# Kernel tuning notes

Measured on AMD Instinct MI355X. Metric: run time of the kernel, lower is better.

## Reference

```python
import jax, jax.numpy as jnp
import numpy as np

DIM, DEPTH, HEADS, DIM_HEAD, MLP = 256, 4, 8, 32, 1024
INNER = HEADS * DIM_HEAD  # 256
B, N = 16, 4096
EPS = 1e-5


def _ln(x, g, b):
    m = jnp.mean(x, axis=-1, keepdims=True)
    v = jnp.mean(jnp.square(x - m), axis=-1, keepdims=True)
    return (x - m) * jax.lax.rsqrt(v + EPS) * g + b


def setup_inputs() -> dict:
    key = jax.random.key(0)
    ks = jax.random.split(key, 16)
    s_in = 1.0 / np.sqrt(DIM)
    s_inner = 1.0 / np.sqrt(INNER)
    s_mlp = 1.0 / np.sqrt(MLP)
    return {
        "x": jax.random.normal(ks[0], (B, N, DIM), jnp.float32),
        "patch_indices": jax.random.randint(ks[1], (B, 2), 0, 64, jnp.int32),
        "data": jnp.zeros((1,), jnp.float32),
        "scale": jnp.array([64, 64], jnp.int32),
        "Wq": jax.random.normal(ks[2], (DEPTH, DIM, INNER), jnp.float32) * s_in,
        "Wk": jax.random.normal(ks[3], (DEPTH, DIM, INNER), jnp.float32) * s_in,
        "Wv": jax.random.normal(ks[4], (DEPTH, DIM, INNER), jnp.float32) * s_in,
        "Wo": jax.random.normal(ks[5], (DEPTH, INNER, DIM), jnp.float32) * s_inner,
        "bo": jnp.zeros((DEPTH, DIM), jnp.float32),
        "ln_g": jnp.ones((DEPTH, DIM), jnp.float32),
        "ln_b": jnp.zeros((DEPTH, DIM), jnp.float32),
        "W1": jax.random.normal(ks[6], (DEPTH, DIM, MLP), jnp.float32) * s_in,
        "b1": jnp.zeros((DEPTH, MLP), jnp.float32),
        "W2": jax.random.normal(ks[7], (DEPTH, MLP, DIM), jnp.float32) * s_mlp,
        "b2": jnp.zeros((DEPTH, DIM), jnp.float32),
        "lnf_g": jnp.ones((DIM,), jnp.float32),
        "lnf_b": jnp.zeros((DIM,), jnp.float32),
    }


def reference(x, patch_indices, data, scale, Wq, Wk, Wv, Wo, bo, ln_g, ln_b,
              W1, b1, W2, b2, lnf_g, lnf_b):
    b, n, dim = x.shape
    attn_scale = DIM_HEAD ** (-0.5)
    # flat index of the center pixel per batch element: row * h_patch + col
    idx = (patch_indices[:, 0] * scale[1] + patch_indices[:, 1]).astype(jnp.int32)  # [b]
    bidx = jnp.arange(b)
    for l in range(DEPTH):
        sel = x[bidx, idx]                                  # [b, dim] gathered center token
        q = (sel @ Wq[l]).reshape(b, HEADS, DIM_HEAD)       # [b, h, d]
        k = (x @ Wk[l]).reshape(b, n, HEADS, DIM_HEAD)      # [b, n, h, d]
        v = (x @ Wv[l]).reshape(b, n, HEADS, DIM_HEAD)
        dots = jnp.einsum('bhd,bnhd->bhn', q, k) * attn_scale
        attn = jax.nn.softmax(dots, axis=-1)                # [b, h, n]
        out = jnp.einsum('bhn,bnhd->bhd', attn, v).reshape(b, INNER)
        out = out @ Wo[l] + bo[l]                           # [b, dim]
        # vectorized scatter of the single attended token back into a zero tensor
        x = jnp.zeros_like(x).at[bidx, idx].set(out) + x
        # FeedForward: LN -> Linear -> GELU (exact) -> Linear, plus residual
        h = jax.nn.gelu(_ln(x, ln_g[l], ln_b[l]) @ W1[l] + b1[l], approximate=False)
        x = h @ W2[l] + b2[l] + x
    return _ln(x, lnf_g, lnf_b)
```

## Files before the change

### kernel.cpp

```cpp
#include <hip/hip_runtime.h>
#include <hip/hip_bf16.h>
#include <math.h>

#define B 16
#define NTOK 4096
#define DIM 256
#define DEPTH 4
#define HEADS 8
#define DH 32
#define INNER 256
#define MLPD 1024
#define EPS 1e-5f

typedef _Float16 half8 __attribute__((ext_vector_type(8)));
typedef _Float16 half4v __attribute__((ext_vector_type(4)));
typedef float f32x4 __attribute__((ext_vector_type(4)));

__device__ __forceinline__ float gelu_fast(float v) {
    const float z = fabsf(v) * 0.70710678118654752440f;
    const float t = __builtin_amdgcn_rcpf(1.f + 0.3275911f * z);
    const float poly = t*(0.254829592f + t*(-0.284496736f +
                      t*(1.421413741f + t*(-1.453152027f + t*1.061405429f))));
    const float e = __expf(-z*z);
    const float erfv = copysignf(1.f - poly * e, v);
    return 0.5f * v * (1.f + erfv);
}

__global__ __launch_bounds__(256) void pack_w(
        const float* __restrict__ in, _Float16* __restrict__ out, int K, int C)
{
    in  += (size_t)blockIdx.z * K * C;
    out += (size_t)blockIdx.z * K * C;
    __shared__ float t[32][65];
    const int tid = threadIdx.x;
    const int c0 = blockIdx.x * 64, k0 = blockIdx.y * 32;
    #pragma unroll
    for (int i = 0; i < 8; ++i) {
        int flat = tid + 256*i;
        int kk = flat >> 6, ccl = flat & 63;
        t[kk][ccl] = in[(size_t)(k0 + kk)*C + c0 + ccl];
    }
    __syncthreads();
    const int lane = tid & 63, ctl = tid >> 6;
    const int ccl = ctl*16 + (lane & 15);
    const int kb = (lane >> 4) * 8;
    half8 v;
    #pragma unroll
    for (int i = 0; i < 8; ++i) v[i] = (_Float16)t[kb + i][ccl];
    size_t off = ((size_t)((c0 >> 4) + ctl) * (K/32) + (k0 >> 5)) * 64 + lane;
    *((half8*)out + off) = v;
}

__global__ __launch_bounds__(256) void attn_prep(
        const float* __restrict__ x, const int* __restrict__ pidx,
        const int* __restrict__ scale,
        const float* __restrict__ Wq, float* __restrict__ qbuf)
{
    const int b = blockIdx.x;
    const int tid = threadIdx.x;
    __shared__ float sel[DIM];
    const int idx = pidx[b*2 + 0] * scale[1] + pidx[b*2 + 1];
    sel[tid] = x[(size_t)b*NTOK*DIM + (size_t)idx*DIM + tid];
    __syncthreads();
    float acc = 0.f;
    #pragma unroll 4
    for (int c = 0; c < DIM; ++c) acc += sel[c] * Wq[c*INNER + tid];
    qbuf[b*DIM + tid] = acc;
}

__global__ __launch_bounds__(256) void qk_kernel(
        const float* __restrict__ qbuf, const float* __restrict__ Wk,
        float* __restrict__ qk)
{
    const int b = blockIdx.y;
    const int tid = threadIdx.x;
    const int wave = tid >> 6, lane = tid & 63;
    __shared__ float qs[DIM];
    qs[tid] = qbuf[b*DIM + tid];
    __syncthreads();
    const float ascale = 0.17677669529663687f;
    const float4 qv = *(const float4*)&qs[lane*4];
    #pragma unroll 4
    for (int i = 0; i < 16; ++i) {
        const int c = blockIdx.x*64 + wave*16 + i;
        const float4 w = *(const float4*)&Wk[(size_t)c*INNER + lane*4];
        float part = w.x*qv.x + w.y*qv.y + w.z*qv.z + w.w*qv.w;
        part += __shfl_xor(part, 1);
        part += __shfl_xor(part, 2);
        part += __shfl_xor(part, 4);
        if ((lane & 7) == 0)
            qk[(b*HEADS + (lane >> 3))*DIM + c] = part * ascale;
    }
}

__global__ __launch_bounds__(256) void dots_kernel(
        const float* __restrict__ x, const float* __restrict__ qk,
        float* __restrict__ dots)
{
    const int b = blockIdx.y;
    const int n0 = blockIdx.x * 32;
    const int tid = threadIdx.x;
    __shared__ float xs[32][260];
    __shared__ float qs[HEADS][260];
    const float4* xg = (const float4*)(x + (size_t)b*NTOK*DIM + (size_t)n0*DIM);
    #pragma unroll
    for (int i = 0; i < 8; ++i) {
        int flat = tid + 256*i;
        int r = flat >> 6, c4 = flat & 63;
        *(float4*)&xs[r][c4*4] = xg[flat];
    }
    const float4* qg = (const float4*)(qk + (size_t)b*HEADS*DIM);
    #pragma unroll
    for (int i = 0; i < 2; ++i) {
        int flat = tid + 256*i;
        int h = flat >> 6, c4 = flat & 63;
        *(float4*)&qs[h][c4*4] = qg[flat];
    }
    __syncthreads();
    const int tok = tid >> 3, h = tid & 7;
    float acc = 0.f;
    #pragma unroll 8
    for (int i = 0; i < 64; ++i) {
        float4 xv = *(const float4*)&xs[tok][i*4];
        float4 qv = *(const float4*)&qs[h][i*4];
        acc += xv.x*qv.x + xv.y*qv.y + xv.z*qv.z + xv.w*qv.w;
    }
    dots[((size_t)(b*HEADS + h))*NTOK + n0 + tok] = acc;
}

__global__ __launch_bounds__(256) void softmax_kernel(float* __restrict__ dots)
{
    float* p = dots + (size_t)blockIdx.x * NTOK;
    const int tid = threadIdx.x;
    float v[16];
    float mx = -3.4e38f;
    #pragma unroll
    for (int i = 0; i < 16; ++i) { v[i] = p[tid + 256*i]; mx = fmaxf(mx, v[i]); }
    #pragma unroll
    for (int o = 32; o > 0; o >>= 1) mx = fmaxf(mx, __shfl_xor(mx, o));
    __shared__ float red[4];
    const int wave = tid >> 6;
    if ((tid & 63) == 0) red[wave] = mx;
    __syncthreads();
    mx = fmaxf(fmaxf(red[0], red[1]), fmaxf(red[2], red[3]));
    float s = 0.f;
    #pragma unroll
    for (int i = 0; i < 16; ++i) { v[i] = __expf(v[i] - mx); s += v[i]; }
    #pragma unroll
    for (int o = 32; o > 0; o >>= 1) s += __shfl_xor(s, o);
    __syncthreads();
    if ((tid & 63) == 0) red[wave] = s;
    __syncthreads();
    s = red[0] + red[1] + red[2] + red[3];
    const float inv = 1.f / s;
    #pragma unroll
    for (int i = 0; i < 16; ++i) p[tid + 256*i] = v[i] * inv;
}

__global__ __launch_bounds__(256) void xa_kernel(
        const float* __restrict__ x, const float* __restrict__ attn,
        float* __restrict__ xa)
{
    const int b = blockIdx.y;
    const int n0 = blockIdx.x * (NTOK/8);
    const int tid = threadIdx.x;
    __shared__ float as[HEADS][NTOK/8];
    const float* ag = attn + (size_t)b*HEADS*NTOK;
    #pragma unroll
    for (int i = 0; i < 16; ++i) {
        int flat = tid + 256*i;
        int h = flat >> 9, n = flat & 511;
        as[h][n] = ag[(size_t)h*NTOK + n0 + n];
    }
    __syncthreads();
    float acc[HEADS];
    #pragma unroll
    for (int h = 0; h < HEADS; ++h) acc[h] = 0.f;
    const float* xg = x + (size_t)b*NTOK*DIM + (size_t)n0*DIM + tid;
    for (int n = 0; n < NTOK/8; ++n) {
        float xv = xg[(size_t)n*DIM];
        #pragma unroll
        for (int h = 0; h < HEADS; ++h) acc[h] += as[h][n] * xv;
    }
    #pragma unroll
    for (int h = 0; h < HEADS; ++h)
        atomicAdd(&xa[(b*HEADS + h)*DIM + tid], acc[h]);
}

__global__ __launch_bounds__(256) void attn_out_kernel(
        const float* __restrict__ xa, const float* __restrict__ Wv,
        const float* __restrict__ Wo, const float* __restrict__ bo,
        const int* __restrict__ pidx, const int* __restrict__ scale,
        float* __restrict__ x)
{
    const int b = blockIdx.x;
    const int tid = threadIdx.x;
    __shared__ float xs[HEADS*DIM];
    __shared__ float vs[INNER];
    #pragma unroll
    for (int i = 0; i < 8; ++i) xs[tid + 256*i] = xa[b*HEADS*DIM + tid + 256*i];
    __syncthreads();
    const int h = tid >> 5;
    float acc = 0.f;
    #pragma unroll 4
    for (int c = 0; c < DIM; ++c) acc += xs[h*DIM + c] * Wv[c*INNER + tid];
    vs[tid] = acc;
    __syncthreads();
    float o = bo[tid];
    #pragma unroll 4
    for (int i = 0; i < INNER; ++i) o += vs[i] * Wo[i*DIM + tid];
    const int idx = pidx[b*2 + 0] * scale[1] + pidx[b*2 + 1];
    x[(size_t)b*NTOK*DIM + (size_t)idx*DIM + tid] += o;
}

__global__ __launch_bounds__(256, 2) void ffn_mfma(
        float* __restrict__ x,
        const float* __restrict__ g, const float* __restrict__ bvec,
        const _Float16* __restrict__ W1F, const float* __restrict__ b1,
        const _Float16* __restrict__ W2F, const float* __restrict__ b2)
{
    __shared__ _Float16 xs[64*256];
    __shared__ _Float16 hsT[64*256];
    const int tid = threadIdx.x;
    const size_t row0 = (size_t)blockIdx.x * 64;

    {
        const int r = tid >> 2, p = tid & 3;
        const float4* xg = (const float4*)(x + (row0 + r)*DIM) + p*16;
        float4 v[16];
        float s = 0.f, s2 = 0.f;
        #pragma unroll
        for (int i = 0; i < 16; ++i) {
            v[i] = xg[i];
            s  += v[i].x + v[i].y + v[i].z + v[i].w;
            s2 += v[i].x*v[i].x + v[i].y*v[i].y + v[i].z*v[i].z + v[i].w*v[i].w;
        }
        s  += __shfl_xor(s, 1);  s  += __shfl_xor(s, 2);
        s2 += __shfl_xor(s2, 1); s2 += __shfl_xor(s2, 2);
        const float mean = s * (1.f/DIM);
        const float rstd = rsqrtf(s2*(1.f/DIM) - mean*mean + EPS);
        #pragma unroll
        for (int q = 0; q < 8; ++q) {
            const int c8 = p*64 + q*8;
            const float4 ga = *(const float4*)&g[c8];
            const float4 gb = *(const float4*)&g[c8+4];
            const float4 ba = *(const float4*)&bvec[c8];
            const float4 bb = *(const float4*)&bvec[c8+4];
            const float4 a = v[2*q], d = v[2*q+1];
            half8 hh;
            hh[0] = (_Float16)((a.x-mean)*rstd*ga.x + ba.x);
            hh[1] = (_Float16)((a.y-mean)*rstd*ga.y + ba.y);
            hh[2] = (_Float16)((a.z-mean)*rstd*ga.z + ba.z);
            hh[3] = (_Float16)((a.w-mean)*rstd*ga.w + ba.w);
            hh[4] = (_Float16)((d.x-mean)*rstd*gb.x + bb.x);
            hh[5] = (_Float16)((d.y-mean)*rstd*gb.y + bb.y);
            hh[6] = (_Float16)((d.z-mean)*rstd*gb.z + bb.z);
            hh[7] = (_Float16)((d.w-mean)*rstd*gb.w + bb.w);
            int byte = r*512 + c8*2;
            byte ^= (r & 7) << 4;
            *(half8*)((char*)xs + byte) = hh;
        }
    }
    __syncthreads();

    const int wave = tid >> 6, lane = tid & 63;
    const int lr = lane & 15, lhi = lane >> 4;

    f32x4 acc2[4][4];
    #pragma unroll
    for (int m = 0; m < 4; ++m)
        #pragma unroll
        for (int n = 0; n < 4; ++n) acc2[m][n] = (f32x4)0.f;

    half8 aA[4], aB[4], bA[4], bB[4];

    for (int cc = 0; cc < 4; ++cc) {
        auto ldA1 = [&](int ks, half8* a) {
            #pragma unroll
            for (int m = 0; m < 4; ++m)
                a[m] = *((const half8*)W1F +
                         (size_t)((cc*16 + wave*4 + m)*8 + ks)*64 + lane);
        };
        auto ldA2 = [&](int ks, half8* a) {
            #pragma unroll
            for (int m = 0; m < 4; ++m)
                a[m] = *((const half8*)W2F +
                         (size_t)((wave*4 + m)*32 + cc*8 + ks)*64 + lane);
        };
        auto ldB = [&](const _Float16* src, int ks, half8* bf) {
            #pragma unroll
            for (int n = 0; n < 4; ++n) {
                int byte = (n*16 + lr)*512 + (ks*32 + lhi*8)*2;
                byte ^= (lr & 7) << 4;
                bf[n] = *(const half8*)((const char*)src + byte);
            }
        };
        auto mm = [&](f32x4 (&acc)[4][4], half8* a, half8* bf) {
            #pragma unroll
            for (int m = 0; m < 4; ++m)
                #pragma unroll
                for (int n = 0; n < 4; ++n)
                    acc[m][n] = __builtin_amdgcn_mfma_f32_16x16x32_f16(
                        a[m], bf[n], acc[m][n], 0, 0, 0);
        };

        f32x4 acc1[4][4];
        #pragma unroll
        for (int m = 0; m < 4; ++m)
            #pragma unroll
            for (int n = 0; n < 4; ++n) acc1[m][n] = (f32x4)0.f;
        ldA1(0, aA); ldB(xs, 0, bA);
        #pragma unroll
        for (int kp = 0; kp < 4; ++kp) {
            ldA1(2*kp+1, aB); ldB(xs, 2*kp+1, bB);
            mm(acc1, aA, bA);
            if (kp < 3) { ldA1(2*kp+2, aA); ldB(xs, 2*kp+2, bA); }
            mm(acc1, aB, bB);
        }
        f32x4 b1r[4];
        #pragma unroll
        for (int m = 0; m < 4; ++m)
            b1r[m] = *(const f32x4*)(b1 + cc*256 + wave*64 + m*16 + lhi*4);
        ldA2(0, aA);
        __syncthreads();
        #pragma unroll
        for (int m = 0; m < 4; ++m) {
            #pragma unroll
            for (int n = 0; n < 4; ++n) {
                const int t = n*16 + lr;
                half4v hv;
                hv[0] = (_Float16)gelu_fast(acc1[m][n][0] + b1r[m][0]);
                hv[1] = (_Float16)gelu_fast(acc1[m][n][1] + b1r[m][1]);
                hv[2] = (_Float16)gelu_fast(acc1[m][n][2] + b1r[m][2]);
                hv[3] = (_Float16)gelu_fast(acc1[m][n][3] + b1r[m][3]);
                int byte = t*512 + (wave*64 + m*16 + lhi*4)*2;
                byte ^= (t & 7) << 4;
                *(half4v*)((char*)hsT + byte) = hv;
            }
        }
        __syncthreads();
        ldB(hsT, 0, bA);
        #pragma unroll
        for (int kp = 0; kp < 4; ++kp) {
            ldA2(2*kp+1, aB); ldB(hsT, 2*kp+1, bB);
            mm(acc2, aA, bA);
            if (kp < 3) { ldA2(2*kp+2, aA); ldB(hsT, 2*kp+2, bA); }
            mm(acc2, aB, bB);
        }
    }
    #pragma unroll
    for (int m = 0; m < 4; ++m) {
        const int c0 = wave*64 + m*16 + lhi*4;
        const f32x4 b2v = *(const f32x4*)(b2 + c0);
        #pragma unroll
        for (int n = 0; n < 4; ++n) {
            const int t = n*16 + lr;
            float* xp = x + (row0 + t)*DIM + c0;
            float4 r = *(const float4*)xp;
            r.x += acc2[m][n][0] + b2v[0];
            r.y += acc2[m][n][1] + b2v[1];
            r.z += acc2[m][n][2] + b2v[2];
            r.w += acc2[m][n][3] + b2v[3];
            *(float4*)xp = r;
        }
    }
}

__global__ __launch_bounds__(256) void final_ln_kernel(
        const float* __restrict__ x, const float* __restrict__ g,
        const float* __restrict__ bvec, float* __restrict__ out)
{
    const int tid = threadIdx.x;
    const size_t row = (size_t)blockIdx.x*32 + (tid >> 3);
    const int p = tid & 7;
    const float4* xr = (const float4*)(x + row*DIM);
    float4 v[8];
    float s = 0.f, s2 = 0.f;
    #pragma unroll
    for (int i = 0; i < 8; ++i) {
        v[i] = xr[p + 8*i];
        s  += v[i].x + v[i].y + v[i].z + v[i].w;
        s2 += v[i].x*v[i].x + v[i].y*v[i].y + v[i].z*v[i].z + v[i].w*v[i].w;
    }
    #pragma unroll
    for (int o = 1; o < 8; o <<= 1) { s += __shfl_xor(s, o); s2 += __shfl_xor(s2, o); }
    const float mean = s * (1.f/DIM);
    const float rstd = rsqrtf(s2*(1.f/DIM) - mean*mean + EPS);
    float4* og = (float4*)(out + row*DIM);
    #pragma unroll
    for (int i = 0; i < 8; ++i) {
        const int c4 = (p + 8*i)*4;
        const float4 gg = *(const float4*)&g[c4];
        const float4 bb = *(const float4*)&bvec[c4];
        float4 o_;
        o_.x = (v[i].x - mean)*rstd*gg.x + bb.x;
        o_.y = (v[i].y - mean)*rstd*gg.y + bb.y;
        o_.z = (v[i].z - mean)*rstd*gg.z + bb.z;
        o_.w = (v[i].w - mean)*rstd*gg.w + bb.w;
        og[p + 8*i] = o_;
    }
}

extern "C" void kernel_launch(void* const* d_in, const int* in_sizes, int n_in,
                              void* d_out, int out_size, void* d_ws, size_t ws_size,
                              hipStream_t stream)
{
    const float* x_in  = (const float*)d_in[0];
    const int*   pidx  = (const int*)d_in[1];
    const int*   scale = (const int*)d_in[3];
    const float* Wq    = (const float*)d_in[4];
    const float* Wk    = (const float*)d_in[5];
    const float* Wv    = (const float*)d_in[6];
    const float* Wo    = (const float*)d_in[7];
    const float* bo    = (const float*)d_in[8];
    const float* ln_g  = (const float*)d_in[9];
    const float* ln_b  = (const float*)d_in[10];
    const float* W1    = (const float*)d_in[11];
    const float* b1    = (const float*)d_in[12];
    const float* W2    = (const float*)d_in[13];
    const float* b2    = (const float*)d_in[14];
    const float* lnf_g = (const float*)d_in[15];
    const float* lnf_b = (const float*)d_in[16];

    float* xbuf = (float*)d_out;
    float* qk   = (float*)d_ws;
    float* dots = qk + (size_t)B*HEADS*DIM;
    float* xa   = dots + (size_t)B*HEADS*NTOK;
    float* qbuf = xa + (size_t)B*HEADS*DIM;
    _Float16* W1F = (_Float16*)(qbuf + (size_t)B*DIM);
    _Float16* W2F = W1F + (size_t)DEPTH*DIM*MLPD;

    pack_w<<<dim3(MLPD/64, DIM/32, DEPTH), 256, 0, stream>>>(W1, W1F, DIM, MLPD);
    pack_w<<<dim3(DIM/64, MLPD/32, DEPTH), 256, 0, stream>>>(W2, W2F, MLPD, DIM);

    hipMemcpyAsync(xbuf, x_in, (size_t)B*NTOK*DIM*sizeof(float),
                   hipMemcpyDeviceToDevice, stream);

    for (int l = 0; l < DEPTH; ++l) {
        attn_prep<<<B, 256, 0, stream>>>(
            xbuf, pidx, scale, Wq + (size_t)l*DIM*INNER, qbuf);
        qk_kernel<<<dim3(4, B), 256, 0, stream>>>(
            qbuf, Wk + (size_t)l*DIM*INNER, qk);
        dots_kernel<<<dim3(NTOK/32, B), 256, 0, stream>>>(xbuf, qk, dots);
        softmax_kernel<<<B*HEADS, 256, 0, stream>>>(dots);
        hipMemsetAsync(xa, 0, (size_t)B*HEADS*DIM*sizeof(float), stream);
        xa_kernel<<<dim3(8, B), 256, 0, stream>>>(xbuf, dots, xa);
        attn_out_kernel<<<B, 256, 0, stream>>>(
            xa, Wv + (size_t)l*DIM*INNER, Wo + (size_t)l*INNER*DIM,
            bo + (size_t)l*DIM, pidx, scale, xbuf);
        ffn_mfma<<<(B*NTOK)/64, 256, 0, stream>>>(
            xbuf, ln_g + (size_t)l*DIM, ln_b + (size_t)l*DIM,
            W1F + (size_t)l*DIM*MLPD, b1 + (size_t)l*MLPD,
            W2F + (size_t)l*MLPD*DIM, b2 + (size_t)l*DIM);
    }
    final_ln_kernel<<<(B*NTOK)/32, 256, 0, stream>>>(xbuf, lnf_g, lnf_b, xbuf);
}
```

Baseline: 1.298 ms.

## Fuse attention into flash-style split pass and halve FFN hidden LDS tile

The separate dots, softmax and attention-weighted sum kernels are replaced by one split-sequence pass that keeps an online-softmax running max and sum per chunk, and a finalize kernel that merges the chunks before the Wv/Wo projection. This removes the round trip of the dots buffer through global memory, the memset and the atomics, and reads x once instead of twice. The q and qk kernels are merged into one launch. The FFN kernel now processes the hidden dimension in 128-wide halves, which halves the hsT shared buffer, raises the launch-bounds occupancy hint to 3 and adds s_setprio around the MFMA calls. The trade-offs are extra block barriers per 32-token step in the attention pass, and the q projection being recomputed by each of the four qk blocks.

Result: slower. 1.888 ms (+45.5%).

```diff
diff --git a/kernel.cpp b/kernel.cpp
--- a/kernel.cpp
+++ b/kernel.cpp
@@ -11,6 +11,8 @@
 #define INNER 256
 #define MLPD 1024
 #define EPS 1e-5f
+#define CH 32
+#define CHTOK (NTOK/CH)
 
 typedef _Float16 half8 __attribute__((ext_vector_type(8)));
 typedef _Float16 half4v __attribute__((ext_vector_type(4)));
@@ -51,32 +53,24 @@
     *((half8*)out + off) = v;
 }
 
-__global__ __launch_bounds__(256) void attn_prep(
+__global__ __launch_bounds__(256) void qk2_kernel(
         const float* __restrict__ x, const int* __restrict__ pidx,
         const int* __restrict__ scale,
-        const float* __restrict__ Wq, float* __restrict__ qbuf)
-{
-    const int b = blockIdx.x;
-    const int tid = threadIdx.x;
+        const float* __restrict__ Wq, const float* __restrict__ Wk,
+        float* __restrict__ qk)
+{
+    const int b = blockIdx.y;
+    const int tid = threadIdx.x;
+    const int wave = tid >> 6, lane = tid & 63;
     __shared__ float sel[DIM];
+    __shared__ float qs[DIM];
     const int idx = pidx[b*2 + 0] * scale[1] + pidx[b*2 + 1];
     sel[tid] = x[(size_t)b*NTOK*DIM + (size_t)idx*DIM + tid];
     __syncthreads();
-    float acc = 0.f;
+    float qacc = 0.f;
     #pragma unroll 4
-    for (int c = 0; c < DIM; ++c) acc += sel[c] * Wq[c*INNER + tid];
-    qbuf[b*DIM + tid] = acc;
-}
-
-__global__ __launch_bounds__(256) void qk_kernel(
-        const float* __restrict__ qbuf, const float* __restrict__ Wk,
-        float* __restrict__ qk)
-{
-    const int b = blockIdx.y;
-    const int tid = threadIdx.x;
-    const int wave = tid >> 6, lane = tid & 63;
-    __shared__ float qs[DIM];
-    qs[tid] = qbuf[b*DIM + tid];
+    for (int c = 0; c < DIM; ++c) qacc += sel[c] * Wq[c*INNER + tid];
+    qs[tid] = qacc;
     __syncthreads();
     const float ascale = 0.17677669529663687f;
     const float4 qv = *(const float4*)&qs[lane*4];
@@ -93,118 +87,130 @@
     }
 }
 
-__global__ __launch_bounds__(256) void dots_kernel(
-        const float* __restrict__ x, const float* __restrict__ qk,
-        float* __restrict__ dots)
-{
-    const int b = blockIdx.y;
-    const int n0 = blockIdx.x * 32;
-    const int tid = threadIdx.x;
+__global__ __launch_bounds__(256) void attn_pass(
+        const float* __restrict__ x, const float* __restrict__ qkg,
+        float* __restrict__ pxa, float* __restrict__ pm, float* __restrict__ ps)
+{
+    const int b = blockIdx.y, ch = blockIdx.x;
+    const int tid = threadIdx.x;
+    __shared__ float qks[HEADS][260];
     __shared__ float xs[32][260];
-    __shared__ float qs[HEADS][260];
-    const float4* xg = (const float4*)(x + (size_t)b*NTOK*DIM + (size_t)n0*DIM);
-    #pragma unroll
-    for (int i = 0; i < 8; ++i) {
-        int flat = tid + 256*i;
-        int r = flat >> 6, c4 = flat & 63;
-        *(float4*)&xs[r][c4*4] = xg[flat];
-    }
-    const float4* qg = (const float4*)(qk + (size_t)b*HEADS*DIM);
+    __shared__ float dotss[32][8];
+    __shared__ float mrun[8], srun[8], mnew_s[8], escale_s[8];
+
+    const float4* qg = (const float4*)(qkg + (size_t)b*HEADS*DIM);
     #pragma unroll
     for (int i = 0; i < 2; ++i) {
         int flat = tid + 256*i;
         int h = flat >> 6, c4 = flat & 63;
-        *(float4*)&qs[h][c4*4] = qg[flat];
-    }
-    __syncthreads();
-    const int tok = tid >> 3, h = tid & 7;
-    float acc = 0.f;
-    #pragma unroll 8
-    for (int i = 0; i < 64; ++i) {
-        float4 xv = *(const float4*)&xs[tok][i*4];
-        float4 qv = *(const float4*)&qs[h][i*4];
-        acc += xv.x*qv.x + xv.y*qv.y + xv.z*qv.z + xv.w*qv.w;
-    }
-    dots[((size_t)(b*HEADS + h))*NTOK + n0 + tok] = acc;
-}
-
-__global__ __launch_bounds__(256) void softmax_kernel(float* __restrict__ dots)
-{
-    float* p = dots + (size_t)blockIdx.x * NTOK;
-    const int tid = threadIdx.x;
-    float v[16];
-    float mx = -3.4e38f;
-    #pragma unroll
-    for (int i = 0; i < 16; ++i) { v[i] = p[tid + 256*i]; mx = fmaxf(mx, v[i]); }
-    #pragma unroll
-    for (int o = 32; o > 0; o >>= 1) mx = fmaxf(mx, __shfl_xor(mx, o));
-    __shared__ float red[4];
-    const int wave = tid >> 6;
-    if ((tid & 63) == 0) red[wave] = mx;
-    __syncthreads();
-    mx = fmaxf(fmaxf(red[0], red[1]), fmaxf(red[2], red[3]));
-    float s = 0.f;
-    #pragma unroll
-    for (int i = 0; i < 16; ++i) { v[i] = __expf(v[i] - mx); s += v[i]; }
-    #pragma unroll
-    for (int o = 32; o > 0; o >>= 1) s += __shfl_xor(s, o);
-    __syncthreads();
-    if ((tid & 63) == 0) red[wave] = s;
-    __syncthreads();
-    s = red[0] + red[1] + red[2] + red[3];
-    const float inv = 1.f / s;
-    #pragma unroll
-    for (int i = 0; i < 16; ++i) p[tid + 256*i] = v[i] * inv;
-}
-
-__global__ __launch_bounds__(256) void xa_kernel(
-        const float* __restrict__ x, const float* __restrict__ attn,
-        float* __restrict__ xa)
-{
-    const int b = blockIdx.y;
-    const int n0 = blockIdx.x * (NTOK/8);
-    const int tid = threadIdx.x;
-    __shared__ float as[HEADS][NTOK/8];
-    const float* ag = attn + (size_t)b*HEADS*NTOK;
-    #pragma unroll
-    for (int i = 0; i < 16; ++i) {
-        int flat = tid + 256*i;
-        int h = flat >> 9, n = flat & 511;
-        as[h][n] = ag[(size_t)h*NTOK + n0 + n];
-    }
-    __syncthreads();
-    float acc[HEADS];
-    #pragma unroll
-    for (int h = 0; h < HEADS; ++h) acc[h] = 0.f;
-    const float* xg = x + (size_t)b*NTOK*DIM + (size_t)n0*DIM + tid;
-    for (int n = 0; n < NTOK/8; ++n) {
-        float xv = xg[(size_t)n*DIM];
-        #pragma unroll
-        for (int h = 0; h < HEADS; ++h) acc[h] += as[h][n] * xv;
-    }
-    #pragma unroll
-    for (int h = 0; h < HEADS; ++h)
-        atomicAdd(&xa[(b*HEADS + h)*DIM + tid], acc[h]);
-}
-
-__global__ __launch_bounds__(256) void attn_out_kernel(
-        const float* __restrict__ xa, const float* __restrict__ Wv,
-        const float* __restrict__ Wo, const float* __restrict__ bo,
-        const int* __restrict__ pidx, const int* __restrict__ scale,
-        float* __restrict__ x)
+        *(float4*)&qks[h][c4*4] = qg[flat];
+    }
+    if (tid < 8) { mrun[tid] = -3.4e38f; srun[tid] = 0.f; }
+    float acc[8];
+    #pragma unroll
+    for (int h = 0; h < 8; ++h) acc[h] = 0.f;
+    __syncthreads();
+
+    for (int st = 0; st < CHTOK/32; ++st) {
+        const size_t n0 = (size_t)ch*CHTOK + st*32;
+        const float4* xg = (const float4*)(x + ((size_t)b*NTOK + n0)*DIM);
+        #pragma unroll
+        for (int i = 0; i < 8; ++i) {
+            int flat = tid + 256*i;
+            int r = flat >> 6, c4 = flat & 63;
+            *(float4*)&xs[r][c4*4] = xg[flat];
+        }
+        __syncthreads();
+        {
+            const int tok = tid >> 3, h = tid & 7;
+            float d = 0.f;
+            #pragma unroll 8
+            for (int i = 0; i < 64; ++i) {
+                float4 xv = *(const float4*)&xs[tok][i*4];
+                float4 qv = *(const float4*)&qks[h][i*4];
+                d += xv.x*qv.x + xv.y*qv.y + xv.z*qv.z + xv.w*qv.w;
+            }
+            dotss[tok][h] = d;
+        }
+        __syncthreads();
+        if (tid < 8) {
+            float tm = -3.4e38f;
+            #pragma unroll
+            for (int n = 0; n < 32; ++n) tm = fmaxf(tm, dotss[n][tid]);
+            const float mo = mrun[tid];
+            const float mn = fmaxf(mo, tm);
+            mnew_s[tid] = mn;
+            escale_s[tid] = __expf(mo - mn);
+        }
+        __syncthreads();
+        {
+            const int tok = tid >> 3, h = tid & 7;
+            dotss[tok][h] = __expf(dotss[tok][h] - mnew_s[h]);
+        }
+        __syncthreads();
+        #pragma unroll
+        for (int h = 0; h < 8; ++h) acc[h] *= escale_s[h];
+        #pragma unroll 4
+        for (int n = 0; n < 32; ++n) {
+            const float xv = xs[n][tid];
+            const float4 w0 = *(const float4*)&dotss[n][0];
+            const float4 w1 = *(const float4*)&dotss[n][4];
+            acc[0] += w0.x*xv; acc[1] += w0.y*xv;
+            acc[2] += w0.z*xv; acc[3] += w0.w*xv;
+            acc[4] += w1.x*xv; acc[5] += w1.y*xv;
+            acc[6] += w1.z*xv; acc[7] += w1.w*xv;
+        }
+        if (tid < 8) {
+            float ts = 0.f;
+            #pragma unroll
+            for (int n = 0; n < 32; ++n) ts += dotss[n][tid];
+            srun[tid] = srun[tid]*escale_s[tid] + ts;
+            mrun[tid] = mnew_s[tid];
+        }
+        __syncthreads();
+    }
+    const size_t base = ((size_t)b*CH + ch)*HEADS;
+    #pragma unroll
+    for (int h = 0; h < 8; ++h)
+        pxa[(base + h)*DIM + tid] = acc[h];
+    if (tid < 8) { pm[base + tid] = mrun[tid]; ps[base + tid] = srun[tid]; }
+}
+
+__global__ __launch_bounds__(256) void attn_fin(
+        const float* __restrict__ pxa, const float* __restrict__ pm,
+        const float* __restrict__ ps,
+        const float* __restrict__ Wv, const float* __restrict__ Wo,
+        const float* __restrict__ bo, const int* __restrict__ pidx,
+        const int* __restrict__ scale, float* __restrict__ x)
 {
     const int b = blockIdx.x;
     const int tid = threadIdx.x;
-    __shared__ float xs[HEADS*DIM];
+    __shared__ float xa_s[HEADS*DIM];
     __shared__ float vs[INNER];
-    #pragma unroll
-    for (int i = 0; i < 8; ++i) xs[tid + 256*i] = xa[b*HEADS*DIM + tid + 256*i];
-    __syncthreads();
-    const int h = tid >> 5;
-    float acc = 0.f;
+
+    #pragma unroll
+    for (int h = 0; h < 8; ++h) {
+        float gm = -3.4e38f;
+        for (int ch = 0; ch < CH; ++ch)
+            gm = fmaxf(gm, pm[((size_t)b*CH + ch)*HEADS + h]);
+        float gs = 0.f;
+        for (int ch = 0; ch < CH; ++ch) {
+            const size_t o = ((size_t)b*CH + ch)*HEADS + h;
+            gs += __expf(pm[o] - gm) * ps[o];
+        }
+        float v = 0.f;
+        for (int ch = 0; ch < CH; ++ch) {
+            const size_t o = ((size_t)b*CH + ch)*HEADS + h;
+            v += __expf(pm[o] - gm) * pxa[o*DIM + tid];
+        }
+        xa_s[h*DIM + tid] = v / gs;
+    }
+    __syncthreads();
+    const int h2 = tid >> 5;
+    float a = 0.f;
     #pragma unroll 4
-    for (int c = 0; c < DIM; ++c) acc += xs[h*DIM + c] * Wv[c*INNER + tid];
-    vs[tid] = acc;
+    for (int c = 0; c < DIM; ++c) a += xa_s[h2*DIM + c] * Wv[c*INNER + tid];
+    vs[tid] = a;
     __syncthreads();
     float o = bo[tid];
     #pragma unroll 4
@@ -213,14 +219,14 @@
     x[(size_t)b*NTOK*DIM + (size_t)idx*DIM + tid] += o;
 }
 
-__global__ __launch_bounds__(256, 2) void ffn_mfma(
+__global__ __launch_bounds__(256, 3) void ffn_mfma(
         float* __restrict__ x,
         const float* __restrict__ g, const float* __restrict__ bvec,
         const _Float16* __restrict__ W1F, const float* __restrict__ b1,
         const _Float16* __restrict__ W2F, const float* __restrict__ b2)
 {
     __shared__ _Float16 xs[64*256];
-    __shared__ _Float16 hsT[64*256];
+    __shared__ _Float16 hsT[64*128];
     const int tid = threadIdx.x;
     const size_t row0 = (size_t)blockIdx.x * 64;
 
@@ -275,77 +281,103 @@
     half8 aA[4], aB[4], bA[4], bB[4];
 
     for (int cc = 0; cc < 4; ++cc) {
-        auto ldA1 = [&](int ks, half8* a) {
-            #pragma unroll
-            for (int m = 0; m < 4; ++m)
-                a[m] = *((const half8*)W1F +
-                         (size_t)((cc*16 + wave*4 + m)*8 + ks)*64 + lane);
-        };
-        auto ldA2 = [&](int ks, half8* a) {
-            #pragma unroll
-            for (int m = 0; m < 4; ++m)
-                a[m] = *((const half8*)W2F +
-                         (size_t)((wave*4 + m)*32 + cc*8 + ks)*64 + lane);
-        };
-        auto ldB = [&](const _Float16* src, int ks, half8* bf) {
-            #pragma unroll
-            for (int n = 0; n < 4; ++n) {
-                int byte = (n*16 + lr)*512 + (ks*32 + lhi*8)*2;
-                byte ^= (lr & 7) << 4;
-                bf[n] = *(const half8*)((const char*)src + byte);
+        #pragma unroll
+        for (int half = 0; half < 2; ++half) {
+            auto ldA1 = [&](int ks, half8* a) {
+                #pragma unroll
+                for (int m = 0; m < 2; ++m)
+                    a[m] = *((const half8*)W1F +
+                        (size_t)((cc*16 + half*8 + m*4 + wave)*8 + ks)*64 + lane);
+            };
+            auto ldBx = [&](int ks, half8* bf) {
+                #pragma unroll
+                for (int n = 0; n < 4; ++n) {
+                    int byte = (n*16 + lr)*512 + (ks*32 + lhi*8)*2;
+                    byte ^= (lr & 7) << 4;
+                    bf[n] = *(const half8*)((const char*)xs + byte);
+                }
+            };
+            auto mm1 = [&](f32x4 (&acc)[2][4], half8* a, half8* bf) {
+                __builtin_amdgcn_s_setprio(1);
+                #pragma unroll
+                for (int m = 0; m < 2; ++m)
+                    #pragma unroll
+                    for (int n = 0; n < 4; ++n)
+                        acc[m][n] = __builtin_amdgcn_mfma_f32_16x16x32_f16(
+                            a[m], bf[n], acc[m][n], 0, 0, 0);
+                __builtin_amdgcn_s_setprio(0);
+            };
+            f32x4 acc1[2][4];
+            #pragma unroll
+            for (int m = 0; m < 2; ++m)
+                #pragma unroll
+                for (int n = 0; n < 4; ++n) acc1[m][n] = (f32x4)0.f;
+            ldA1(0, aA); ldBx(0, bA);
+            #pragma unroll
+            for (int kp = 0; kp < 4; ++kp) {
+                ldA1(2*kp+1, aB); ldBx(2*kp+1, bB);
+                mm1(acc1, aA, bA);
+                if (kp < 3) { ldA1(2*kp+2, aA); ldBx(2*kp+2, bA); }
+                mm1(acc1, aB, bB);
             }
-        };
-        auto mm = [&](f32x4 (&acc)[4][4], half8* a, half8* bf) {
-            #pragma unroll
-            for (int m = 0; m < 4; ++m)
-                #pragma unroll
-                for (int n = 0; n < 4; ++n)
-                    acc[m][n] = __builtin_amdgcn_mfma_f32_16x16x32_f16(
-                        a[m], bf[n], acc[m][n], 0, 0, 0);
-        };
-
-        f32x4 acc1[4][4];
-        #pragma unroll
-        for (int m = 0; m < 4; ++m)
-            #pragma unroll
-            for (int n = 0; n < 4; ++n) acc1[m][n] = (f32x4)0.f;
-        ldA1(0, aA); ldB(xs, 0, bA);
-        #pragma unroll
-        for (int kp = 0; kp < 4; ++kp) {
-            ldA1(2*kp+1, aB); ldB(xs, 2*kp+1, bB);
-            mm(acc1, aA, bA);
-            if (kp < 3) { ldA1(2*kp+2, aA); ldB(xs, 2*kp+2, bA); }
-            mm(acc1, aB, bB);
-        }
-        f32x4 b1r[4];
-        #pragma unroll
-        for (int m = 0; m < 4; ++m)
-            b1r[m] = *(const f32x4*)(b1 + cc*256 + wave*64 + m*16 + lhi*4);
-        ldA2(0, aA);
-        __syncthreads();
-        #pragma unroll
-        for (int m = 0; m < 4; ++m) {
-            #pragma unroll
-            for (int n = 0; n < 4; ++n) {
-                const int t = n*16 + lr;
-                half4v hv;
-                hv[0] = (_Float16)gelu_fast(acc1[m][n][0] + b1r[m][0]);
-                hv[1] = (_Float16)gelu_fast(acc1[m][n][1] + b1r[m][1]);
-                hv[2] = (_Float16)gelu_fast(acc1[m][n][2] + b1r[m][2]);
-                hv[3] = (_Float16)gelu_fast(acc1[m][n][3] + b1r[m][3]);
-                int byte = t*512 + (wave*64 + m*16 + lhi*4)*2;
-                byte ^= (t & 7) << 4;
-                *(half4v*)((char*)hsT + byte) = hv;
+            f32x4 b1r[2];
+            #pragma unroll
+            for (int m = 0; m < 2; ++m)
+                b1r[m] = *(const f32x4*)(b1 + cc*256 + half*128 +
+                                         (m*4 + wave)*16 + lhi*4);
+            auto ldA2 = [&](int ks2, half8* a) {
+                const int kb = cc*8 + half*4 + ks2;
+                #pragma unroll
+                for (int m = 0; m < 4; ++m)
+                    a[m] = *((const half8*)W2F +
+                        (size_t)((wave*4 + m)*32 + kb)*64 + lane);
+            };
+            ldA2(0, aA);
+            __syncthreads();
+            #pragma unroll
+            for (int m = 0; m < 2; ++m) {
+                const int c_local = (m*4 + wave)*16 + lhi*4;
+                #pragma unroll
+                for (int n = 0; n < 4; ++n) {
+                    const int t = n*16 + lr;
+                    half4v hv;
+                    hv[0] = (_Float16)gelu_fast(acc1[m][n][0] + b1r[m][0]);
+                    hv[1] = (_Float16)gelu_fast(acc1[m][n][1] + b1r[m][1]);
+                    hv[2] = (_Float16)gelu_fast(acc1[m][n][2] + b1r[m][2]);
+                    hv[3] = (_Float16)gelu_fast(acc1[m][n][3] + b1r[m][3]);
+                    int byte = t*256 + c_local*2;
+                    byte ^= (t & 7) << 4;
+                    *(half4v*)((char*)hsT + byte) = hv;
+                }
             }
-        }
-        __syncthreads();
-        ldB(hsT, 0, bA);
-        #pragma unroll
-        for (int kp = 0; kp < 4; ++kp) {
-            ldA2(2*kp+1, aB); ldB(hsT, 2*kp+1, bB);
-            mm(acc2, aA, bA);
-            if (kp < 3) { ldA2(2*kp+2, aA); ldB(hsT, 2*kp+2, bA); }
-            mm(acc2, aB, bB);
+            __syncthreads();
+            auto ldBh = [&](int ks2, half8* bf) {
+                #pragma unroll
+                for (int n = 0; n < 4; ++n) {
+                    const int t = n*16 + lr;
+                    int byte = t*256 + (ks2*32 + lhi*8)*2;
+                    byte ^= (t & 7) << 4;
+                    bf[n] = *(const half8*)((const char*)hsT + byte);
+                }
+            };
+            auto mm2 = [&](half8* a, half8* bf) {
+                __builtin_amdgcn_s_setprio(1);
+                #pragma unroll
+                for (int m = 0; m < 4; ++m)
+                    #pragma unroll
+                    for (int n = 0; n < 4; ++n)
+                        acc2[m][n] = __builtin_amdgcn_mfma_f32_16x16x32_f16(
+                            a[m], bf[n], acc2[m][n], 0, 0, 0);
+                __builtin_amdgcn_s_setprio(0);
+            };
+            ldBh(0, bA);
+            ldA2(1, aB); ldBh(1, bB);
+            mm2(aA, bA);
+            ldA2(2, aA); ldBh(2, bA);
+            mm2(aB, bB);
+            ldA2(3, aB); ldBh(3, bB);
+            mm2(aA, bA);
+            mm2(aB, bB);
         }
     }
     #pragma unroll
@@ -424,10 +456,10 @@
 
     float* xbuf = (float*)d_out;
     float* qk   = (float*)d_ws;
-    float* dots = qk + (size_t)B*HEADS*DIM;
-    float* xa   = dots + (size_t)B*HEADS*NTOK;
-    float* qbuf = xa + (size_t)B*HEADS*DIM;
-    _Float16* W1F = (_Float16*)(qbuf + (size_t)B*DIM);
+    float* pxa  = qk + (size_t)B*HEADS*DIM;
+    float* pm   = pxa + (size_t)B*CH*HEADS*DIM;
+    float* ps   = pm + (size_t)B*CH*HEADS;
+    _Float16* W1F = (_Float16*)(ps + (size_t)B*CH*HEADS);
     _Float16* W2F = W1F + (size_t)DEPTH*DIM*MLPD;
 
     pack_w<<<dim3(MLPD/64, DIM/32, DEPTH), 256, 0, stream>>>(W1, W1F, DIM, MLPD);
@@ -437,16 +469,12 @@
                    hipMemcpyDeviceToDevice, stream);
 
     for (int l = 0; l < DEPTH; ++l) {
-        attn_prep<<<B, 256, 0, stream>>>(
-            xbuf, pidx, scale, Wq + (size_t)l*DIM*INNER, qbuf);
-        qk_kernel<<<dim3(4, B), 256, 0, stream>>>(
-            qbuf, Wk + (size_t)l*DIM*INNER, qk);
-        dots_kernel<<<dim3(NTOK/32, B), 256, 0, stream>>>(xbuf, qk, dots);
-        softmax_kernel<<<B*HEADS, 256, 0, stream>>>(dots);
-        hipMemsetAsync(xa, 0, (size_t)B*HEADS*DIM*sizeof(float), stream);
-        xa_kernel<<<dim3(8, B), 256, 0, stream>>>(xbuf, dots, xa);
-        attn_out_kernel<<<B, 256, 0, stream>>>(
-            xa, Wv + (size_t)l*DIM*INNER, Wo + (size_t)l*INNER*DIM,
+        qk2_kernel<<<dim3(4, B), 256, 0, stream>>>(
+            xbuf, pidx, scale,
+            Wq + (size_t)l*DIM*INNER, Wk + (size_t)l*DIM*INNER, qk);
+        attn_pass<<<dim3(CH, B), 256, 0, stream>>>(xbuf, qk, pxa, pm, ps);
+        attn_fin<<<B, 256, 0, stream>>>(
+            pxa, pm, ps, Wv + (size_t)l*DIM*INNER, Wo + (size_t)l*INNER*DIM,
             bo + (size_t)l*DIM, pidx, scale, xbuf);
         ffn_mfma<<<(B*NTOK)/64, 256, 0, stream>>>(
             xbuf, ln_g + (size_t)l*DIM, ln_b + (size_t)l*DIM,
```
